# Kernel tuning notes

Hardware: AMD Instinct MI355X
Metric: run time of the kernel (lower is better)

Reference implementation:

```python
import jax, jax.numpy as jnp
import numpy as np

EPS = 1e-9
N, E = 100000, 1000000
IN_F, OUT_F, HEADS = 128, 64, 2


def normalize_points(x):
    # UHG projective normalize: unit-norm spatial part, keep last (homogeneous) coord
    n = jnp.linalg.norm(x[..., :-1], axis=-1, keepdims=True)
    return jnp.concatenate([x[..., :-1] / jnp.maximum(n, EPS), x[..., -1:]], axis=-1)


def uhg_inner(a, b):
    # hyperbolic inner product: spatial dot minus time-time product
    return jnp.sum(a[..., :-1] * b[..., :-1], axis=-1) - a[..., -1] * b[..., -1]


def compute_cross_ratio(p1, p2, p3, p4):
    num = uhg_inner(p1, p3) * uhg_inner(p2, p4)
    den = uhg_inner(p1, p4) * uhg_inner(p2, p3)
    return num / jnp.where(jnp.abs(den) < EPS, EPS, den)


def restore_cross_ratio(x, cr_target):
    cr_cur = compute_cross_ratio(x[0], x[1], x[2], x[3])
    scale = jnp.abs(cr_target / jnp.where(jnp.abs(cr_cur) < EPS, EPS, cr_cur)) ** 0.25
    return x * scale


def setup_inputs() -> dict:
    key = jax.random.key(0)
    ks = jax.random.split(key, 10)
    s_in = 1.0 / np.sqrt(IN_F)
    s_hid = 1.0 / np.sqrt(OUT_F * HEADS)
    H = OUT_F * HEADS
    return {
        "x": jax.random.normal(ks[0], (N, IN_F), dtype=jnp.float32),
        "edge_index": jax.random.randint(ks[1], (2, E), 0, N, dtype=jnp.int64),
        "Wq": jax.random.uniform(ks[2], (H, IN_F), jnp.float32, -s_in, s_in),
        "bq": jnp.zeros((H,), jnp.float32),
        "Wk": jax.random.uniform(ks[3], (H, IN_F), jnp.float32, -s_in, s_in),
        "bk": jnp.zeros((H,), jnp.float32),
        "Wv": jax.random.uniform(ks[4], (H, IN_F), jnp.float32, -s_in, s_in),
        "bv": jnp.zeros((H,), jnp.float32),
        "Wo": jax.random.uniform(ks[5], (OUT_F, H), jnp.float32, -s_hid, s_hid),
        "bo": jnp.zeros((OUT_F,), jnp.float32),
    }


def reference(x, edge_index, Wq, bq, Wk, bk, Wv, bv, Wo, bo):
    n = x.shape[0]
    cr_initial = compute_cross_ratio(x[0], x[1], x[2], x[3])
    x_proj = normalize_points(x)
    q = (x_proj @ Wq.T + bq).reshape(n, HEADS, OUT_F)
    k = (x_proj @ Wk.T + bk).reshape(n, HEADS, OUT_F)
    v = (x_proj @ Wv.T + bv).reshape(n, HEADS, OUT_F)
    row, col = edge_index[0], edge_index[1]
    qe = normalize_points(q[row])  # [E, H, D]
    ke = normalize_points(k[col])
    scores = uhg_inner(qe, ke) / np.sqrt(IN_F)  # [E, H]
    alpha = jax.nn.softmax(scores, axis=0)  # global softmax over edges (as in source)
    msgs = v[col] * alpha[..., None]  # [E, H, D]
    out = jax.ops.segment_sum(msgs, row, num_segments=n)  # [N, H, D]
    out = out.reshape(n, HEADS * OUT_F)
    out = out @ Wo.T + bo
    out = restore_cross_ratio(out, cr_initial)
    return out
```

## Files before the change

### kernel.cpp

```cpp
#include <hip/hip_runtime.h>
#include <math.h>

#define EPSF 1e-9f
#define INV_SQRT128 0.08838834764831845f

typedef _Float16 half8 __attribute__((ext_vector_type(8)));
typedef _Float16 half4v __attribute__((ext_vector_type(4)));
typedef float f32x4 __attribute__((ext_vector_type(4)));

__device__ __forceinline__ void gl_lds16(const void* g, void* l) {
    __builtin_amdgcn_global_load_lds((const __attribute__((address_space(1))) void*)g,
                                     (__attribute__((address_space(3))) void*)l, 16, 0, 0);
}

__global__ void k_wpack(const float* __restrict__ Wq, const float* __restrict__ Wk,
                        const float* __restrict__ Wv, half8* __restrict__ whi,
                        half8* __restrict__ wlo, float* __restrict__ w127) {
    int t = blockIdx.x * 256 + threadIdx.x;
    if (t >= 6144) return;
    int col = t & 127, g = (t >> 7) & 3, ks = (t >> 9) & 3, kind = t >> 11;
    const float* W = (kind == 0) ? Wq : (kind == 1) ? Wk : Wv;
    const float4* W4 = (const float4*)W;
    float4 a = W4[col * 32 + ks * 8 + g * 2];
    float4 b = W4[col * 32 + ks * 8 + g * 2 + 1];
    float xv[8] = {a.x, a.y, a.z, a.w, b.x, b.y, b.z, b.w};
    half8 h, lo;
#pragma unroll
    for (int j = 0; j < 8; j++) {
        _Float16 hh = (_Float16)xv[j];
        h[j] = hh;
        lo[j] = (_Float16)((xv[j] - (float)hh) * 4096.0f);
    }
    whi[t] = h;
    wlo[t] = lo;
    if (ks == 3 && g == 3) w127[kind * 128 + col] = xv[7];
}

__global__ void k_wpack2(const float* __restrict__ Wo, half8* __restrict__ wohi,
                         half8* __restrict__ wolo) {
    int t = blockIdx.x * 256 + threadIdx.x;
    if (t >= 1024) return;
    int col = t & 63, g = (t >> 6) & 3, ks = t >> 8;
    const float4* W4 = (const float4*)Wo;
    float4 a = W4[col * 32 + ks * 8 + g * 2];
    float4 b = W4[col * 32 + ks * 8 + g * 2 + 1];
    float xv[8] = {a.x, a.y, a.z, a.w, b.x, b.y, b.z, b.w};
    half8 h, lo;
#pragma unroll
    for (int j = 0; j < 8; j++) {
        _Float16 hh = (_Float16)xv[j];
        h[j] = hh;
        lo[j] = (_Float16)((xv[j] - (float)hh) * 4096.0f);
    }
    wohi[t] = h;
    wolo[t] = lo;
}

__global__ void __launch_bounds__(256, 2)
k_qkvm(const float* __restrict__ x,
       const half8* __restrict__ whi, const half8* __restrict__ wlo,
       const float* __restrict__ w127,
       const float* __restrict__ bq, const float* __restrict__ bk,
       const float* __restrict__ bv,
       float* __restrict__ qn, _Float16* __restrict__ knh, float* __restrict__ vn,
       const int* __restrict__ ei, int* __restrict__ bcnt,
       int N, int E, int chunk) {
    int b = (int)blockIdx.x;
    __shared__ half8 bsh[4096];
    if (b < 512 && (b & 1)) {
        int* h = (int*)bsh;
        int t = threadIdx.x;
        int hid = b >> 1;
        h[t] = 0;
        __syncthreads();
        int s = hid * chunk, e1 = min(s + chunk, E);
        for (int e = s + t; e < e1; e += 256) atomicAdd(&h[ei[e] >> 9], 1);
        __syncthreads();
        bcnt[hid * 256 + t] = h[t];
        return;
    }
    int gb = (b < 512) ? (b >> 1) : (b - 256);

    int tid = threadIdx.x;
    int wv = tid >> 6;
    int l = tid & 63;
    int r = l & 15;
    int g = l >> 4;
    int rowbase = gb * 128 + wv * 32;
    const float4* x4 = (const float4*)x;

    {
        const half8* sH = whi + wv * 512;
        const half8* sL = wlo + wv * 512;
#pragma unroll
        for (int i = 0; i < 8; i++) {
            gl_lds16(sH + i * 64 + l, bsh + wv * 512 + i * 64);
            gl_lds16(sL + i * 64 + l, bsh + 2048 + wv * 512 + i * 64);
        }
    }

    half8 hiA[2][4], loA[2][4];
    float rnj[2][4], tcj[2][4];
#pragma unroll
    for (int t = 0; t < 2; t++) {
        int row = min(rowbase + t * 16 + r, N - 1);
        float ssum = 0.f, tl = 0.f;
#pragma unroll
        for (int ks = 0; ks < 4; ks++) {
            float4 a = x4[(size_t)row * 32 + ks * 8 + g * 2];
            float4 bb = x4[(size_t)row * 32 + ks * 8 + g * 2 + 1];
            float xv[8] = {a.x, a.y, a.z, a.w, bb.x, bb.y, bb.z, bb.w};
#pragma unroll
            for (int j = 0; j < 8; j++) {
                _Float16 hh = (_Float16)xv[j];
                hiA[t][ks][j] = hh;
                loA[t][ks][j] = (_Float16)((xv[j] - (float)hh) * 4096.0f);
                ssum += xv[j] * xv[j];
            }
            if (ks == 3 && g == 3) { tl = xv[7]; ssum -= xv[7] * xv[7]; }
        }
        ssum += __shfl_xor(ssum, 16);
        ssum += __shfl_xor(ssum, 32);
        float rn = 1.f / fmaxf(sqrtf(ssum), EPSF);
        float tla = __shfl(tl, 48 + r);
        float tc = tla * (1.f - rn);
#pragma unroll
        for (int j = 0; j < 4; j++) {
            rnj[t][j] = __shfl(rn, g * 4 + j);
            tcj[t][j] = __shfl(tc, g * 4 + j);
        }
    }

    asm volatile("s_waitcnt vmcnt(0)" ::: "memory");
    __syncthreads();

    const float* const bks[3] = {bq, bk, bv};
    bool lane15 = (r == 15);
    const f32x4 zz = {0.f, 0.f, 0.f, 0.f};
    int dsbase = g * 128 + r;

#pragma unroll
    for (int kind = 0; kind < 3; kind++) {
        float wcA[2][4], bbA[2][4];
#pragma unroll
        for (int h = 0; h < 2; h++)
#pragma unroll
            for (int ct = 0; ct < 4; ct++) {
                int col = (h * 4 + ct) * 16 + r;
                wcA[h][ct] = w127[kind * 128 + col];
                bbA[h][ct] = bks[kind][col];
            }

#pragma unroll
        for (int h = 0; h < 2; h++) {
            f32x4 aM[2][4], aX[2][4];
#pragma unroll
            for (int t = 0; t < 2; t++)
#pragma unroll
                for (int ct = 0; ct < 4; ct++) { aM[t][ct] = zz; aX[t][ct] = zz; }

#pragma unroll
            for (int ks = 0; ks < 4; ks++) {
                half8 hB[4], lB[4];
#pragma unroll
                for (int ct = 0; ct < 4; ct++) {
                    int bi = dsbase + ks * 512 + (h * 4 + ct) * 16;
                    hB[ct] = bsh[bi];
                    lB[ct] = bsh[2048 + bi];
                }
#pragma unroll
                for (int ct = 0; ct < 4; ct++) {
                    aM[0][ct] = __builtin_amdgcn_mfma_f32_16x16x32_f16(hiA[0][ks], hB[ct], aM[0][ct], 0, 0, 0);
                    aM[1][ct] = __builtin_amdgcn_mfma_f32_16x16x32_f16(hiA[1][ks], hB[ct], aM[1][ct], 0, 0, 0);
                    aX[0][ct] = __builtin_amdgcn_mfma_f32_16x16x32_f16(hiA[0][ks], lB[ct], aX[0][ct], 0, 0, 0);
                    aX[0][ct] = __builtin_amdgcn_mfma_f32_16x16x32_f16(loA[0][ks], hB[ct], aX[0][ct], 0, 0, 0);
                    aX[1][ct] = __builtin_amdgcn_mfma_f32_16x16x32_f16(hiA[1][ks], lB[ct], aX[1][ct], 0, 0, 0);
                    aX[1][ct] = __builtin_amdgcn_mfma_f32_16x16x32_f16(loA[1][ks], hB[ct], aX[1][ct], 0, 0, 0);
                }
            }

            if (h == 1 && kind < 2) {
                __syncthreads();
                const half8* sH = whi + (kind + 1) * 2048 + wv * 512;
                const half8* sL = wlo + (kind + 1) * 2048 + wv * 512;
#pragma unroll
                for (int i = 0; i < 8; i++) {
                    gl_lds16(sH + i * 64 + l, bsh + wv * 512 + i * 64);
                    gl_lds16(sL + i * 64 + l, bsh + 2048 + wv * 512 + i * 64);
                }
            }

#pragma unroll
            for (int t = 0; t < 2; t++) {
                float cv[4][4];
#pragma unroll
                for (int ct = 0; ct < 4; ct++)
#pragma unroll
                    for (int j = 0; j < 4; j++) {
                        float acc = aM[t][ct][j] + aX[t][ct][j] * (1.0f / 4096.0f);
                        cv[ct][j] = fmaf(rnj[t][j], acc, fmaf(tcj[t][j], wcA[h][ct], bbA[h][ct]));
                    }
                if (kind < 2) {
#pragma unroll
                    for (int j = 0; j < 4; j++) {
                        float ss = 0.f;
#pragma unroll
                        for (int ct = 0; ct < 4; ct++) {
                            float c = cv[ct][j];
                            ss += (ct == 3 && lane15) ? 0.f : c * c;
                        }
                        ss += __shfl_xor(ss, 1);
                        ss += __shfl_xor(ss, 2);
                        ss += __shfl_xor(ss, 4);
                        ss += __shfl_xor(ss, 8);
                        float rh = 1.f / fmaxf(sqrtf(ss), EPSF);
#pragma unroll
                        for (int ct = 0; ct < 4; ct++) {
                            bool ist = (ct == 3) && lane15;
                            if (!ist) cv[ct][j] *= rh;
                            if (kind == 0) {
                                if (ist) cv[ct][j] = -cv[ct][j];
                                cv[ct][j] *= INV_SQRT128;
                            }
                        }
                    }
                }
#pragma unroll
                for (int j = 0; j < 4; j++) {
                    int row = rowbase + t * 16 + g * 4 + j;
                    if (row < N) {
                        if (kind == 0) {
                            float* dst = qn + (size_t)row * 128;
#pragma unroll
                            for (int ct = 0; ct < 4; ct++)
                                dst[(h * 4 + ct) * 16 + r] = cv[ct][j];
                        } else if (kind == 1) {
                            _Float16* dst = knh + (size_t)row * 128;
#pragma unroll
                            for (int ct = 0; ct < 4; ct++)
                                dst[(h * 4 + ct) * 16 + r] = (_Float16)cv[ct][j];
                        } else {
                            float* dst = vn + (size_t)row * 128;
#pragma unroll
                            for (int ct = 0; ct < 4; ct++)
                                dst[(h * 4 + ct) * 16 + r] = cv[ct][j];
                        }
                    }
                }
            }
        }

        if (kind < 2) {
            asm volatile("s_waitcnt vmcnt(0)" ::: "memory");
            __syncthreads();
        }
    }
}

__global__ void k_bin2(int* __restrict__ bcnt, int* __restrict__ bintot) {
    __shared__ int sd[256];
    int b = blockIdx.x, t = threadIdx.x;
    int v = bcnt[t * 256 + b];
    sd[t] = v;
    __syncthreads();
    for (int off = 1; off < 256; off <<= 1) {
        int val = sd[t];
        int add = (t >= off) ? sd[t - off] : 0;
        __syncthreads();
        sd[t] = val + add;
        __syncthreads();
    }
    bcnt[t * 256 + b] = sd[t] - v;
    if (t == 255) bintot[b] = sd[255];
}

__global__ void k_bin3(const int* __restrict__ bintot, int* __restrict__ binoff,
                       int* __restrict__ offs, int N, int E) {
    __shared__ int sd[256];
    int t = threadIdx.x;
    int v = bintot[t];
    sd[t] = v;
    __syncthreads();
    for (int off = 1; off < 256; off <<= 1) {
        int val = sd[t];
        int add = (t >= off) ? sd[t - off] : 0;
        __syncthreads();
        sd[t] = val + add;
        __syncthreads();
    }
    binoff[t] = sd[t] - v;
    if (t == 255) {
        binoff[256] = sd[255];
        offs[N] = E;
    }
}

__global__ void k_scat1(const int* __restrict__ ei, const int* __restrict__ bcnt,
                        const int* __restrict__ binoff, int* __restrict__ packed,
                        int E, int chunk) {
    __shared__ int cur[256];
    int t = threadIdx.x, b = blockIdx.x;
    cur[t] = binoff[t] + bcnt[b * 256 + t];
    __syncthreads();
    int s = b * chunk, e1 = min(s + chunk, E);
    for (int e = s + t; e < e1; e += 256) {
        int r = ei[e];
        int c = ei[E + e];
        int p = atomicAdd(&cur[r >> 9], 1);
        packed[p] = ((r & 511) << 17) | c;
    }
}

__global__ void __launch_bounds__(256)
k_sortf(const int* __restrict__ packed, const int* __restrict__ binoff,
        int* __restrict__ ccol, int* __restrict__ offs, int N) {
    __shared__ int seg[6656];
    __shared__ int h[512];
    __shared__ int sc[256];
    int b = blockIdx.x, t = threadIdx.x;
    int s = binoff[b], e1 = binoff[b + 1];
    int cnt = min(e1 - s, 6656);
    for (int i = t; i < cnt; i += 256) seg[i] = packed[s + i];
    h[t] = 0;
    h[t + 256] = 0;
    __syncthreads();
    for (int i = t; i < cnt; i += 256) atomicAdd(&h[seg[i] >> 17], 1);
    __syncthreads();
    int v0 = h[2 * t], v1 = h[2 * t + 1];
    int pair = v0 + v1;
    sc[t] = pair;
    __syncthreads();
    for (int off = 1; off < 256; off <<= 1) {
        int val = sc[t];
        int add = (t >= off) ? sc[t - off] : 0;
        __syncthreads();
        sc[t] = val + add;
        __syncthreads();
    }
    int pexcl = sc[t] - pair;
    __syncthreads();
    h[2 * t] = pexcl;
    h[2 * t + 1] = pexcl + v0;
    int rowbase = b << 9;
    if (rowbase + 2 * t < N) offs[rowbase + 2 * t] = s + h[2 * t];
    if (rowbase + 2 * t + 1 < N) offs[rowbase + 2 * t + 1] = s + h[2 * t + 1];
    __syncthreads();
    for (int i = t; i < cnt; i += 256) {
        int pk = seg[i];
        int p = atomicAdd(&h[pk >> 17], 1);
        ccol[s + p] = pk & 0x1FFFF;
    }
}

__global__ void k_score(const float* __restrict__ qn, const _Float16* __restrict__ knh,
                        const int* __restrict__ offs, const int* __restrict__ ccol,
                        float* __restrict__ e2, double* __restrict__ psum, int N, int E) {
    int g = threadIdx.x >> 5;
    int l = threadIdx.x & 31;
    int head = l >> 4;
    int n = blockIdx.x * 8 + g;
    double esum = 0.0;
    if (n < N) {
        float4 q4 = ((const float4*)qn)[(size_t)n * 32 + l];
        int s0 = offs[n], s1 = offs[n + 1];
        const half4v* k4p = (const half4v*)knh;
        float* eh = e2 + (size_t)head * E;
        int i = s0;
        for (; i + 4 <= s1; i += 4) {
            int c0 = ccol[i];
            int c1 = ccol[i + 1];
            int c2 = ccol[i + 2];
            int c3 = ccol[i + 3];
            half4v ka = k4p[(size_t)c0 * 32 + l];
            half4v kb = k4p[(size_t)c1 * 32 + l];
            half4v kc = k4p[(size_t)c2 * 32 + l];
            half4v kd = k4p[(size_t)c3 * 32 + l];
            float p0 = q4.x * (float)ka[0];
            p0 = fmaf(q4.y, (float)ka[1], p0); p0 = fmaf(q4.z, (float)ka[2], p0);
            p0 = fmaf(q4.w, (float)ka[3], p0);
            float p1 = q4.x * (float)kb[0];
            p1 = fmaf(q4.y, (float)kb[1], p1); p1 = fmaf(q4.z, (float)kb[2], p1);
            p1 = fmaf(q4.w, (float)kb[3], p1);
            float p2 = q4.x * (float)kc[0];
            p2 = fmaf(q4.y, (float)kc[1], p2); p2 = fmaf(q4.z, (float)kc[2], p2);
            p2 = fmaf(q4.w, (float)kc[3], p2);
            float p3 = q4.x * (float)kd[0];
            p3 = fmaf(q4.y, (float)kd[1], p3); p3 = fmaf(q4.z, (float)kd[2], p3);
            p3 = fmaf(q4.w, (float)kd[3], p3);
            p0 += __shfl_xor(p0, 1); p1 += __shfl_xor(p1, 1);
            p2 += __shfl_xor(p2, 1); p3 += __shfl_xor(p3, 1);
            p0 += __shfl_xor(p0, 2); p1 += __shfl_xor(p1, 2);
            p2 += __shfl_xor(p2, 2); p3 += __shfl_xor(p3, 2);
            p0 += __shfl_xor(p0, 4); p1 += __shfl_xor(p1, 4);
            p2 += __shfl_xor(p2, 4); p3 += __shfl_xor(p3, 4);
            p0 += __shfl_xor(p0, 8); p1 += __shfl_xor(p1, 8);
            p2 += __shfl_xor(p2, 8); p3 += __shfl_xor(p3, 8);
            float x0 = expf(p0);
            float x1 = expf(p1);
            float x2 = expf(p2);
            float x3 = expf(p3);
            if ((l & 15) == 0) {
                eh[i] = x0;
                eh[i + 1] = x1;
                eh[i + 2] = x2;
                eh[i + 3] = x3;
                esum += (double)((x0 + x1) + (x2 + x3));
            }
        }
        for (; i < s1; i++) {
            int c = ccol[i];
            half4v k4 = k4p[(size_t)c * 32 + l];
            float p = q4.x * (float)k4[0];
            p = fmaf(q4.y, (float)k4[1], p); p = fmaf(q4.z, (float)k4[2], p);
            p = fmaf(q4.w, (float)k4[3], p);
            p += __shfl_xor(p, 1);
            p += __shfl_xor(p, 2);
            p += __shfl_xor(p, 4);
            p += __shfl_xor(p, 8);
            float xx = expf(p);
            if ((l & 15) == 0) {
                eh[i] = xx;
                esum += (double)xx;
            }
        }
    }
    __shared__ double sd[2][8];
    if ((l & 15) == 0) sd[head][g] = esum;
    __syncthreads();
    if (threadIdx.x < 2) {
        double s = 0.0;
        for (int i2 = 0; i2 < 8; i2++) s += sd[threadIdx.x][i2];
        psum[(size_t)blockIdx.x * 2 + threadIdx.x] = s;
    }
}

__global__ void k_aggr(const float* __restrict__ vn, const int* __restrict__ offs,
                       const int* __restrict__ ccol, const float* __restrict__ e2,
                       float* __restrict__ U, int N, int E) {
    int g = threadIdx.x >> 5;
    int l = threadIdx.x & 31;
    int head = l >> 4;
    int n = blockIdx.x * 8 + g;
    if (n >= N) return;
    int s0 = offs[n], s1 = offs[n + 1];
    const float4* v4p = (const float4*)vn;
    const float* eh = e2 + (size_t)head * E;
    float4 acc = {0.f, 0.f, 0.f, 0.f};
    int i = s0;
    for (; i + 4 <= s1; i += 4) {
        int c0 = ccol[i];
        int c1 = ccol[i + 1];
        int c2 = ccol[i + 2];
        int c3 = ccol[i + 3];
        float4 va = v4p[(size_t)c0 * 32 + l];
        float4 vb = v4p[(size_t)c1 * 32 + l];
        float4 vc = v4p[(size_t)c2 * 32 + l];
        float4 vd = v4p[(size_t)c3 * 32 + l];
        float x0 = eh[i];
        float x1 = eh[i + 1];
        float x2 = eh[i + 2];
        float x3 = eh[i + 3];
        acc.x = fmaf(va.x, x0, acc.x); acc.y = fmaf(va.y, x0, acc.y);
        acc.z = fmaf(va.z, x0, acc.z); acc.w = fmaf(va.w, x0, acc.w);
        acc.x = fmaf(vb.x, x1, acc.x); acc.y = fmaf(vb.y, x1, acc.y);
        acc.z = fmaf(vb.z, x1, acc.z); acc.w = fmaf(vb.w, x1, acc.w);
        acc.x = fmaf(vc.x, x2, acc.x); acc.y = fmaf(vc.y, x2, acc.y);
        acc.z = fmaf(vc.z, x2, acc.z); acc.w = fmaf(vc.w, x2, acc.w);
        acc.x = fmaf(vd.x, x3, acc.x); acc.y = fmaf(vd.y, x3, acc.y);
        acc.z = fmaf(vd.z, x3, acc.z); acc.w = fmaf(vd.w, x3, acc.w);
    }
    for (; i < s1; i++) {
        int c = ccol[i];
        float4 v4 = v4p[(size_t)c * 32 + l];
        float xx = eh[i];
        acc.x = fmaf(v4.x, xx, acc.x); acc.y = fmaf(v4.y, xx, acc.y);
        acc.z = fmaf(v4.z, xx, acc.z); acc.w = fmaf(v4.w, xx, acc.w);
    }
    ((float4*)U)[(size_t)n * 32 + l] = acc;
}

__global__ void k_crout4(const float* __restrict__ x, const float* __restrict__ U,
                         const float* __restrict__ Wo, const float* __restrict__ bo,
                         const double* __restrict__ psum, int P,
                         double* __restrict__ sumf, float* __restrict__ scalef) {
    __shared__ float xs[4 * 128];
    __shared__ float o4[4 * 64];
    __shared__ double crin_sh;
    __shared__ double sdr[2][4];
    int tid = threadIdx.x;
    {
        double s0 = 0.0, s1 = 0.0;
        for (int i = tid; i < P; i += 256) {
            s0 += psum[2 * i];
            s1 += psum[2 * i + 1];
        }
        for (int off = 32; off; off >>= 1) {
            s0 += __shfl_xor(s0, off);
            s1 += __shfl_xor(s1, off);
        }
        int w = tid >> 6;
        if ((tid & 63) == 0) { sdr[0][w] = s0; sdr[1][w] = s1; }
    }
    xs[tid] = U[tid];
    xs[tid + 256] = U[tid + 256];
    __syncthreads();
    if (tid == 0) {
        double s0 = sdr[0][0] + sdr[0][1] + sdr[0][2] + sdr[0][3];
        double s1 = sdr[1][0] + sdr[1][1] + sdr[1][2] + sdr[1][3];
        sumf[0] = s0;
        sumf[1] = s1;
    }
    if (tid >= 64 && tid < 128) {
        int l = tid - 64;
        const int pa[4] = {0, 1, 0, 1};
        const int pb[4] = {2, 3, 3, 2};
        double inner[4];
        for (int p = 0; p < 4; p++) {
            const float* a = x + pa[p] * 128;
            const float* b = x + pb[p] * 128;
            double s = (double)a[l] * (double)b[l];
            double t = (double)a[l + 64] * (double)b[l + 64];
            s += (l == 63) ? -t : t;
            for (int off = 32; off; off >>= 1) s += __shfl_xor(s, off);
            inner[p] = s;
        }
        if (l == 0) {
            double num = inner[0] * inner[1];
            double den = inner[2] * inner[3];
            if (fabs(den) < 1e-9) den = 1e-9;
            crin_sh = num / den;
        }
    }
    __syncthreads();
    int w = tid >> 6, o = tid & 63;
    float si0 = (float)(1.0 / sumf[0]);
    float si1 = (float)(1.0 / sumf[1]);
    const float* xr = xs + w * 128;
    const float* wr = Wo + (size_t)o * 128;
    float d0 = 0.f, d1 = 0.f;
    for (int j = 0; j < 64; j++) d0 = fmaf(xr[j], wr[j], d0);
    for (int j = 64; j < 128; j++) d1 = fmaf(xr[j], wr[j], d1);
    o4[w * 64 + o] = d0 * si0 + d1 * si1 + bo[o];
    __syncthreads();
    if (tid < 64) {
        int l = tid;
        const int pa[4] = {0, 1, 0, 1};
        const int pb[4] = {2, 3, 3, 2};
        double inner[4];
        for (int p = 0; p < 4; p++) {
            double t = (double)o4[pa[p] * 64 + l] * (double)o4[pb[p] * 64 + l];
            if (l == 63) t = -t;
            for (int off = 32; off; off >>= 1) t += __shfl_xor(t, off);
            inner[p] = t;
        }
        if (l == 0) {
            double num = inner[0] * inner[1];
            double den = inner[2] * inner[3];
            if (fabs(den) < 1e-9) den = 1e-9;
            double crc = num / den;
            if (fabs(crc) < 1e-9) crc = 1e-9;
            double ratio = crin_sh / crc;
            scalef[0] = (float)pow(fabs(ratio), 0.25);
        }
    }
}

__global__ void __launch_bounds__(256, 2)
k_outm(const float* __restrict__ U, const half8* __restrict__ wohi,
       const half8* __restrict__ wolo, const float* __restrict__ bo,
       const double* __restrict__ sumf, const float* __restrict__ scalef,
       float* __restrict__ out, int N) {
    __shared__ half8 bsh[2048];
    int tid = threadIdx.x;
    int wv = tid >> 6;
    int l = tid & 63;
    int r = l & 15;
    int g = l >> 4;
    int rowbase = blockIdx.x * 128 + wv * 32;

    {
        const half8* sH = wohi + wv * 256;
        const half8* sL = wolo + wv * 256;
#pragma unroll
        for (int i = 0; i < 4; i++) {
            gl_lds16(sH + i * 64 + l, bsh + wv * 256 + i * 64);
            gl_lds16(sL + i * 64 + l, bsh + 1024 + wv * 256 + i * 64);
        }
    }

    float si0 = (float)(1.0 / sumf[0]);
    float si1 = (float)(1.0 / sumf[1]);
    const float4* U4 = (const float4*)U;
    half8 hiA[2][4], loA[2][4];
#pragma unroll
    for (int t = 0; t < 2; t++) {
        int row = min(rowbase + t * 16 + r, N - 1);
#pragma unroll
        for (int ks = 0; ks < 4; ks++) {
            float si = (ks < 2) ? si0 : si1;
            float4 a = U4[(size_t)row * 32 + ks * 8 + g * 2];
            float4 b = U4[(size_t)row * 32 + ks * 8 + g * 2 + 1];
            float xv[8] = {a.x, a.y, a.z, a.w, b.x, b.y, b.z, b.w};
#pragma unroll
            for (int j = 0; j < 8; j++) {
                float v = xv[j] * si;
                _Float16 hh = (_Float16)v;
                hiA[t][ks][j] = hh;
                loA[t][ks][j] = (_Float16)((v - (float)hh) * 4096.0f);
            }
        }
    }

    asm volatile("s_waitcnt vmcnt(0)" ::: "memory");
    __syncthreads();

    const f32x4 zz = {0.f, 0.f, 0.f, 0.f};
    f32x4 aM[2][4], aX[2][4];
#pragma unroll
    for (int t = 0; t < 2; t++)
#pragma unroll
        for (int ct = 0; ct < 4; ct++) { aM[t][ct] = zz; aX[t][ct] = zz; }

#pragma unroll
    for (int ks = 0; ks < 4; ks++) {
        half8 hB[4], lB[4];
#pragma unroll
        for (int ct = 0; ct < 4; ct++) {
            int bi = ks * 256 + g * 64 + ct * 16 + r;
            hB[ct] = bsh[bi];
            lB[ct] = bsh[1024 + bi];
        }
#pragma unroll
        for (int ct = 0; ct < 4; ct++) {
            aM[0][ct] = __builtin_amdgcn_mfma_f32_16x16x32_f16(hiA[0][ks], hB[ct], aM[0][ct], 0, 0, 0);
            aM[1][ct] = __builtin_amdgcn_mfma_f32_16x16x32_f16(hiA[1][ks], hB[ct], aM[1][ct], 0, 0, 0);
            aX[0][ct] = __builtin_amdgcn_mfma_f32_16x16x32_f16(hiA[0][ks], lB[ct], aX[0][ct], 0, 0, 0);
            aX[0][ct] = __builtin_amdgcn_mfma_f32_16x16x32_f16(loA[0][ks], hB[ct], aX[0][ct], 0, 0, 0);
            aX[1][ct] = __builtin_amdgcn_mfma_f32_16x16x32_f16(hiA[1][ks], lB[ct], aX[1][ct], 0, 0, 0);
            aX[1][ct] = __builtin_amdgcn_mfma_f32_16x16x32_f16(loA[1][ks], hB[ct], aX[1][ct], 0, 0, 0);
        }
    }

    float sf = scalef[0];
#pragma unroll
    for (int t = 0; t < 2; t++)
#pragma unroll
        for (int ct = 0; ct < 4; ct++) {
            float bb = bo[ct * 16 + r];
#pragma unroll
            for (int j = 0; j < 4; j++) {
                int row = rowbase + t * 16 + g * 4 + j;
                if (row < N) {
                    float c = (aM[t][ct][j] + aX[t][ct][j] * (1.0f / 4096.0f) + bb) * sf;
                    out[(size_t)row * 64 + ct * 16 + r] = c;
                }
            }
        }
}

extern "C" void kernel_launch(void* const* d_in, const int* in_sizes, int n_in,
                              void* d_out, int out_size, void* d_ws, size_t ws_size,
                              hipStream_t stream) {
    const float* x  = (const float*)d_in[0];
    const int*   ei = (const int*)d_in[1];
    const float* Wq = (const float*)d_in[2];
    const float* bq = (const float*)d_in[3];
    const float* Wk = (const float*)d_in[4];
    const float* bk = (const float*)d_in[5];
    const float* Wv = (const float*)d_in[6];
    const float* bv = (const float*)d_in[7];
    const float* Wo = (const float*)d_in[8];
    const float* bo = (const float*)d_in[9];
    float* out = (float*)d_out;

    const int N = in_sizes[0] / 128;
    const int E = in_sizes[1] / 2;
    const size_t NR = (size_t)N * 128;
    const int NGB = (N + 127) / 128;
    const int GB = (N + 7) / 8;
    const int chunk = (E + 255) / 256;
    const int NBINS = (N + 511) >> 9;

    float* qn = (float*)d_ws;
    float* vn = qn + NR;
    _Float16* knh = (_Float16*)(vn + NR);
    int* offs = (int*)(knh + NR);
    int* ccol = offs + N + 2;
    int* bcnt = ccol + E;
    int* bintot = bcnt + 256 * 256;
    int* binoff = bintot + 256;
    uintptr_t pe = ((uintptr_t)(binoff + 257 + 1) + 15) & ~(uintptr_t)15;
    float* e2 = (float*)pe;
    uintptr_t pd = ((uintptr_t)(e2 + 2 * (size_t)E) + 7) & ~(uintptr_t)7;
    double* psum = (double*)pd;
    double* sumf = psum + (size_t)GB * 2;
    float* scalef = (float*)(sumf + 2);

    uintptr_t pw = ((uintptr_t)ccol + 15) & ~(uintptr_t)15;
    half8* whi = (half8*)pw;
    half8* wlo = whi + 6144;
    float* w127 = (float*)(wlo + 6144);

    uintptr_t pw2 = ((uintptr_t)bcnt + 15) & ~(uintptr_t)15;
    half8* wohi = (half8*)pw2;
    half8* wolo = wohi + 1024;

    float* U = qn;

    k_wpack<<<24, 256, 0, stream>>>(Wq, Wk, Wv, whi, wlo, w127);
    k_qkvm<<<NGB + 256, 256, 0, stream>>>(x, whi, wlo, w127, bq, bk, bv,
                                          qn, knh, vn, ei, bcnt, N, E, chunk);
    k_bin2<<<256, 256, 0, stream>>>(bcnt, bintot);
    k_bin3<<<1, 256, 0, stream>>>(bintot, binoff, offs, N, E);
    k_scat1<<<256, 256, 0, stream>>>(ei, bcnt, binoff, ccol, E, chunk);
    k_wpack2<<<4, 256, 0, stream>>>(Wo, wohi, wolo);
    k_sortf<<<NBINS, 256, 0, stream>>>(ccol, binoff, ccol, offs, N);
    k_score<<<GB, 256, 0, stream>>>(qn, knh, offs, ccol, e2, psum, N, E);
    k_aggr<<<GB, 256, 0, stream>>>(vn, offs, ccol, e2, U, N, E);
    k_crout4<<<1, 256, 0, stream>>>(x, U, Wo, bo, psum, GB, sumf, scalef);
    k_outm<<<NGB, 256, 0, stream>>>(U, wohi, wolo, bo, sumf, scalef, out, N);
}
```

Measured before the change: 382.1 us.

## Halve QKV weight LDS buffer and stage per head-half to raise occupancy

The packed weight layout now groups each 64-column head-half contiguously, so the QKV projection kernel keeps only half the weights in LDS at a time (64KB down to 32KB). Weights are reloaded six times per block, one per (kind, head) phase, instead of three. Launch bounds are raised from 2 to 4 blocks per CU to hide memory latency better. The cost is more barriers and more frequent weight reloads, plus register pressure that the tighter launch bound may turn into spills.

Result: slower. 472.4 us (+23.6%).

```diff
diff --git a/kernel.cpp b/kernel.cpp
--- a/kernel.cpp
+++ b/kernel.cpp
@@ -18,20 +18,21 @@
                         half8* __restrict__ wlo, float* __restrict__ w127) {
     int t = blockIdx.x * 256 + threadIdx.x;
     if (t >= 6144) return;
-    int col = t & 127, g = (t >> 7) & 3, ks = (t >> 9) & 3, kind = t >> 11;
+    int colp = t & 63, g = (t >> 6) & 3, ks = (t >> 8) & 3, h = (t >> 10) & 1, kind = t >> 11;
+    int col = h * 64 + colp;
     const float* W = (kind == 0) ? Wq : (kind == 1) ? Wk : Wv;
     const float4* W4 = (const float4*)W;
     float4 a = W4[col * 32 + ks * 8 + g * 2];
     float4 b = W4[col * 32 + ks * 8 + g * 2 + 1];
     float xv[8] = {a.x, a.y, a.z, a.w, b.x, b.y, b.z, b.w};
-    half8 h, lo;
+    half8 hh8, lo;
 #pragma unroll
     for (int j = 0; j < 8; j++) {
         _Float16 hh = (_Float16)xv[j];
-        h[j] = hh;
+        hh8[j] = hh;
         lo[j] = (_Float16)((xv[j] - (float)hh) * 4096.0f);
     }
-    whi[t] = h;
+    whi[t] = hh8;
     wlo[t] = lo;
     if (ks == 3 && g == 3) w127[kind * 128 + col] = xv[7];
 }
@@ -56,7 +57,7 @@
     wolo[t] = lo;
 }
 
-__global__ void __launch_bounds__(256, 2)
+__global__ void __launch_bounds__(256, 4)
 k_qkvm(const float* __restrict__ x,
        const half8* __restrict__ whi, const half8* __restrict__ wlo,
        const float* __restrict__ w127,
@@ -66,7 +67,7 @@
        const int* __restrict__ ei, int* __restrict__ bcnt,
        int N, int E, int chunk) {
     int b = (int)blockIdx.x;
-    __shared__ half8 bsh[4096];
+    __shared__ half8 bsh[2048];
     if (b < 512 && (b & 1)) {
         int* h = (int*)bsh;
         int t = threadIdx.x;
@@ -90,12 +91,12 @@
     const float4* x4 = (const float4*)x;
 
     {
-        const half8* sH = whi + wv * 512;
-        const half8* sL = wlo + wv * 512;
-#pragma unroll
-        for (int i = 0; i < 8; i++) {
-            gl_lds16(sH + i * 64 + l, bsh + wv * 512 + i * 64);
-            gl_lds16(sL + i * 64 + l, bsh + 2048 + wv * 512 + i * 64);
+        const half8* sH = whi + wv * 256;
+        const half8* sL = wlo + wv * 256;
+#pragma unroll
+        for (int i = 0; i < 4; i++) {
+            gl_lds16(sH + i * 64 + l, bsh + wv * 256 + i * 64);
+            gl_lds16(sL + i * 64 + l, bsh + 1024 + wv * 256 + i * 64);
         }
     }
 
@@ -137,22 +138,21 @@
     const float* const bks[3] = {bq, bk, bv};
     bool lane15 = (r == 15);
     const f32x4 zz = {0.f, 0.f, 0.f, 0.f};
-    int dsbase = g * 128 + r;
+    int dsb = g * 64 + r;
 
 #pragma unroll
     for (int kind = 0; kind < 3; kind++) {
-        float wcA[2][4], bbA[2][4];
-#pragma unroll
-        for (int h = 0; h < 2; h++)
+#pragma unroll
+        for (int h = 0; h < 2; h++) {
+            int ph = kind * 2 + h;
+            float wcA[4], bbA[4];
 #pragma unroll
             for (int ct = 0; ct < 4; ct++) {
                 int col = (h * 4 + ct) * 16 + r;
-                wcA[h][ct] = w127[kind * 128 + col];
-                bbA[h][ct] = bks[kind][col];
-            }
-
-#pragma unroll
-        for (int h = 0; h < 2; h++) {
+                wcA[ct] = w127[kind * 128 + col];
+                bbA[ct] = bks[kind][col];
+            }
+
             f32x4 aM[2][4], aX[2][4];
 #pragma unroll
             for (int t = 0; t < 2; t++)
@@ -164,9 +164,9 @@
                 half8 hB[4], lB[4];
 #pragma unroll
                 for (int ct = 0; ct < 4; ct++) {
-                    int bi = dsbase + ks * 512 + (h * 4 + ct) * 16;
+                    int bi = ks * 256 + dsb + ct * 16;
                     hB[ct] = bsh[bi];
-                    lB[ct] = bsh[2048 + bi];
+                    lB[ct] = bsh[1024 + bi];
                 }
 #pragma unroll
                 for (int ct = 0; ct < 4; ct++) {
@@ -179,14 +179,14 @@
                 }
             }
 
-            if (h == 1 && kind < 2) {
+            if (ph < 5) {
                 __syncthreads();
-                const half8* sH = whi + (kind + 1) * 2048 + wv * 512;
-                const half8* sL = wlo + (kind + 1) * 2048 + wv * 512;
-#pragma unroll
-                for (int i = 0; i < 8; i++) {
-                    gl_lds16(sH + i * 64 + l, bsh + wv * 512 + i * 64);
-                    gl_lds16(sL + i * 64 + l, bsh + 2048 + wv * 512 + i * 64);
+                const half8* sH = whi + (ph + 1) * 1024 + wv * 256;
+                const half8* sL = wlo + (ph + 1) * 1024 + wv * 256;
+#pragma unroll
+                for (int i = 0; i < 4; i++) {
+                    gl_lds16(sH + i * 64 + l, bsh + wv * 256 + i * 64);
+                    gl_lds16(sL + i * 64 + l, bsh + 1024 + wv * 256 + i * 64);
                 }
             }
 
@@ -198,7 +198,7 @@
 #pragma unroll
                     for (int j = 0; j < 4; j++) {
                         float acc = aM[t][ct][j] + aX[t][ct][j] * (1.0f / 4096.0f);
-                        cv[ct][j] = fmaf(rnj[t][j], acc, fmaf(tcj[t][j], wcA[h][ct], bbA[h][ct]));
+                        cv[ct][j] = fmaf(rnj[t][j], acc, fmaf(tcj[t][j], wcA[ct], bbA[ct]));
                     }
                 if (kind < 2) {
 #pragma unroll
@@ -248,11 +248,11 @@
                     }
                 }
             }
-        }
-
-        if (kind < 2) {
-            asm volatile("s_waitcnt vmcnt(0)" ::: "memory");
-            __syncthreads();
+
+            if (ph < 5) {
+                asm volatile("s_waitcnt vmcnt(0)" ::: "memory");
+                __syncthreads();
+            }
         }
     }
 }
```
